# Performance work log

Measured on AMD Instinct MI355X. Metric: run time of the kernel, lower is better.

The kernel has to match this reference:

```python
import jax, jax.numpy as jnp
import numpy as np

B, T, I, H, O = 8192, 128, 28, 200, 10


def setup_inputs() -> dict:
    key = jax.random.key(0)
    ks = jax.random.split(key, 7)
    s_ih = 1.0 / np.sqrt(H)
    return {
        "x": jax.random.normal(ks[0], (B, T, I), dtype=jnp.float32),
        "W_ih": jax.random.uniform(ks[1], (H, I), jnp.float32, -s_ih, s_ih),
        "W_hh": jax.random.uniform(ks[2], (H, H), jnp.float32, -s_ih, s_ih),
        "b_ih": jax.random.uniform(ks[3], (H,), jnp.float32, -s_ih, s_ih),
        "b_hh": jax.random.uniform(ks[4], (H,), jnp.float32, -s_ih, s_ih),
        "W_fc": jax.random.uniform(ks[5], (O, H), jnp.float32, -s_ih, s_ih),
        "b_fc": jax.random.uniform(ks[6], (O,), jnp.float32, -s_ih, s_ih),
    }


def reference(x, W_ih, W_hh, b_ih, b_hh, W_fc, b_fc):
    # Precompute input projections for all timesteps in one GEMM: [B,T,H]
    xp = jnp.einsum("bti,hi->bth", x, W_ih) + b_ih + b_hh
    h0 = jnp.zeros((x.shape[0], W_hh.shape[0]), dtype=x.dtype)

    def step(h, xp_t):
        # h_t = relu(x_t W_ih^T + b_ih + h_{t-1} W_hh^T + b_hh)
        h = jax.nn.relu(xp_t + h @ W_hh.T)
        return h, None

    # scan over time: xp transposed to [T,B,H]
    h_last, _ = jax.lax.scan(step, h0, jnp.swapaxes(xp, 0, 1))
    # out[:, -1, :] then fc1
    return h_last @ W_fc.T + b_fc
```

## Files before the change

### kernel.cpp

```cpp
#include <hip/hip_runtime.h>
#include <hip/hip_bf16.h>

typedef float f4v __attribute__((ext_vector_type(4)));
typedef short s8v __attribute__((ext_vector_type(8)));

#define TT 128
#define II 28
#define HH 200
#define BB 16
#define NT 128
#define SH 232
#define KX 224
#define SF 212

__device__ __forceinline__ int pk_bf16(float a, float b) {
    union { __hip_bfloat162 h; int i; } u;
    u.h = __float22bfloat162_rn(make_float2(a, b));
    return u.i;
}
__device__ __forceinline__ short f2bf(float f) {
    union { __hip_bfloat16 h; short s; } u;
    u.h = __float2bfloat16(f);
    return u.s;
}

__global__ __launch_bounds__(NT, 1)
void rnn_w2(const float* __restrict__ x,
            const float* __restrict__ W_ih,
            const float* __restrict__ W_hh,
            const float* __restrict__ b_ih,
            const float* __restrict__ b_hh,
            const float* __restrict__ W_fc,
            const float* __restrict__ b_fc,
            float* __restrict__ out)
{
    __shared__ __align__(16) short Hs[2][BB][SH];
    __shared__ __align__(16) float Hf[BB][SF];

    const int tid  = threadIdx.x;
    const int lane = tid & 63;
    const int q    = lane >> 4;
    const int lr   = lane & 15;
    const int wave = tid >> 6;
    const int b0   = blockIdx.x * BB;

    const int first = wave * 7;
    const int cnt   = wave ? 6 : 7;

    for (int i = tid; i < 2 * BB * SH / 2; i += NT) ((int*)Hs)[i] = 0;

    s8v Af[7][8];
    #pragma unroll
    for (int u = 0; u < 7; ++u) {
        const int j = 16 * (first + u) + lr;
        #pragma unroll
        for (int kc = 0; kc < 8; ++kc) {
            union { short s[8]; s8v v; } tv;
            #pragma unroll
            for (int i = 0; i < 8; ++i) {
                const int k = 32 * kc + 8 * q + i;
                float w = 0.0f;
                if (u < cnt && j < HH) {
                    if (k < HH)                    w = W_hh[j * HH + k];
                    else if (k >= KX && k < KX+II) w = W_ih[j * II + (k - KX)];
                }
                tv.s[i] = f2bf(w);
            }
            Af[u][kc] = tv.v;
        }
    }

    f4v biasv[7];
    #pragma unroll
    for (int u = 0; u < 7; ++u) {
        f4v bv = {0.f, 0.f, 0.f, 0.f};
        #pragma unroll
        for (int i = 0; i < 4; ++i) {
            const int j = 16 * (first + u) + 4 * q + i;
            if (u < cnt && j < HH) bv[i] = b_ih[j] + b_hh[j];
        }
        biasv[u] = bv;
    }

    const float* xp = x + (long)(b0 + lr) * (TT * II) + 8 * q;
    f4v xa0 = {0,0,0,0}, xb0 = {0,0,0,0}, xa1 = {0,0,0,0}, xb1 = {0,0,0,0};
    xa0 = *(const f4v*)(xp);
    if (q != 3) xb0 = *(const f4v*)(xp + 4);
    xa1 = *(const f4v*)(xp + II);
    if (q != 3) xb1 = *(const f4v*)(xp + II + 4);

    __syncthreads();

    auto step = [&](int t, int pb, f4v& xa, f4v& xb) {
        union { int i4[4]; s8v v; } xf;
        xf.i4[0] = pk_bf16(xa.x, xa.y);
        xf.i4[1] = pk_bf16(xa.z, xa.w);
        xf.i4[2] = pk_bf16(xb.x, xb.y);
        xf.i4[3] = pk_bf16(xb.z, xb.w);
        {
            const int tn = (t + 2 < TT) ? t + 2 : TT - 1;
            xa = *(const f4v*)(xp + tn * II);
            if (q != 3) xb = *(const f4v*)(xp + tn * II + 4);
        }

        s8v bf[7];
        #pragma unroll
        for (int kc = 0; kc < 7; ++kc)
            bf[kc] = *(const s8v*)&Hs[pb][lr][32 * kc + 8 * q];

        #pragma unroll
        for (int u = 0; u < 7; ++u) {
            if (u < cnt) {
                const int jt = first + u;
                f4v acc = __builtin_amdgcn_mfma_f32_16x16x32_bf16(Af[u][7], xf.v, biasv[u], 0, 0, 0);
                #pragma unroll
                for (int kc = 0; kc < 7; ++kc)
                    acc = __builtin_amdgcn_mfma_f32_16x16x32_bf16(Af[u][kc], bf[kc], acc, 0, 0, 0);

                const float r0 = fmaxf(acc.x, 0.f), r1 = fmaxf(acc.y, 0.f);
                const float r2 = fmaxf(acc.z, 0.f), r3 = fmaxf(acc.w, 0.f);
                int2 hv;
                hv.x = pk_bf16(r0, r1);
                hv.y = pk_bf16(r2, r3);
                *(int2*)&Hs[pb ^ 1][lr][16 * jt + 4 * q] = hv;
                if (t == TT - 1) {
                    f4v rf = {r0, r1, r2, r3};
                    *(f4v*)&Hf[lr][16 * jt + 4 * q] = rf;
                }
            }
        }
        __syncthreads();
    };

    for (int tb = 0; tb < TT; tb += 2) {
        step(tb,     0, xa0, xb0);
        step(tb + 1, 1, xa1, xb1);
    }

    for (int i = tid; i < BB * 10; i += NT) {
        const int o = i >> 4, r = i & 15;
        float s = b_fc[o];
        for (int k = 0; k < HH; ++k)
            s = fmaf(Hf[r][k], W_fc[o * HH + k], s);
        __builtin_nontemporal_store(s, &out[(long)(b0 + r) * 10 + o]);
    }
}

extern "C" void kernel_launch(void* const* d_in, const int* in_sizes, int n_in,
                              void* d_out, int out_size, void* d_ws, size_t ws_size,
                              hipStream_t stream) {
    const float* x    = (const float*)d_in[0];
    const float* W_ih = (const float*)d_in[1];
    const float* W_hh = (const float*)d_in[2];
    const float* b_ih = (const float*)d_in[3];
    const float* b_hh = (const float*)d_in[4];
    const float* W_fc = (const float*)d_in[5];
    const float* b_fc = (const float*)d_in[6];
    float* out = (float*)d_out;

    rnn_w2<<<dim3(8192 / BB), dim3(NT), 0, stream>>>(
        x, W_ih, W_hh, b_ih, b_hh, W_fc, b_fc, out);
}
```

Measured before the change: 325.4 us.

## Interleave independent MFMA chains and prefetch x four timesteps ahead

The MFMA loop is reordered so that the seven output tiles' accumulators advance together across k-chunks, replacing seven serial dependent chains per tile. This hides MFMA latency between dependent instructions. The x prefetch changes from a 2-step lookahead to chunked 4-timestep double buffering, so global load latency is covered over several steps. Wave 1 now always computes the seventh tile, which is padding with zero weights, and simply skips storing it. This trades extra MFMA work and more registers for fewer stalls.

```diff
diff --git a/kernel.cpp b/kernel.cpp
--- a/kernel.cpp
+++ b/kernel.cpp
@@ -25,7 +25,7 @@
 }
 
 __global__ __launch_bounds__(NT, 1)
-void rnn_w2(const float* __restrict__ x,
+void rnn_w3(const float* __restrict__ x,
             const float* __restrict__ W_ih,
             const float* __restrict__ W_hh,
             const float* __restrict__ b_ih,
@@ -45,7 +45,6 @@
     const int b0   = blockIdx.x * BB;
 
     const int first = wave * 7;
-    const int cnt   = wave ? 6 : 7;
 
     for (int i = tid; i < 2 * BB * SH / 2; i += NT) ((int*)Hs)[i] = 0;
 
@@ -60,7 +59,7 @@
             for (int i = 0; i < 8; ++i) {
                 const int k = 32 * kc + 8 * q + i;
                 float w = 0.0f;
-                if (u < cnt && j < HH) {
+                if (j < HH) {
                     if (k < HH)                    w = W_hh[j * HH + k];
                     else if (k >= KX && k < KX+II) w = W_ih[j * II + (k - KX)];
                 }
@@ -77,48 +76,50 @@
         #pragma unroll
         for (int i = 0; i < 4; ++i) {
             const int j = 16 * (first + u) + 4 * q + i;
-            if (u < cnt && j < HH) bv[i] = b_ih[j] + b_hh[j];
+            if (j < HH) bv[i] = b_ih[j] + b_hh[j];
         }
         biasv[u] = bv;
     }
 
     const float* xp = x + (long)(b0 + lr) * (TT * II) + 8 * q;
-    f4v xa0 = {0,0,0,0}, xb0 = {0,0,0,0}, xa1 = {0,0,0,0}, xb1 = {0,0,0,0};
-    xa0 = *(const f4v*)(xp);
-    if (q != 3) xb0 = *(const f4v*)(xp + 4);
-    xa1 = *(const f4v*)(xp + II);
-    if (q != 3) xb1 = *(const f4v*)(xp + II + 4);
+    f4v xA[8] = {}, xB[8] = {};
+    #pragma unroll
+    for (int s = 0; s < 4; ++s) {
+        xA[2*s] = *(const f4v*)(xp + s * II);
+        if (q < 3) xA[2*s+1] = *(const f4v*)(xp + s * II + 4);
+    }
 
     __syncthreads();
 
-    auto step = [&](int t, int pb, f4v& xa, f4v& xb) {
+    auto step = [&](int t, int pb, const f4v& xa, const f4v& xb) {
+        s8v bf[7];
+        #pragma unroll
+        for (int kc = 0; kc < 7; ++kc)
+            bf[kc] = *(const s8v*)&Hs[pb][lr][32 * kc + 8 * q];
+
         union { int i4[4]; s8v v; } xf;
         xf.i4[0] = pk_bf16(xa.x, xa.y);
         xf.i4[1] = pk_bf16(xa.z, xa.w);
         xf.i4[2] = pk_bf16(xb.x, xb.y);
         xf.i4[3] = pk_bf16(xb.z, xb.w);
-        {
-            const int tn = (t + 2 < TT) ? t + 2 : TT - 1;
-            xa = *(const f4v*)(xp + tn * II);
-            if (q != 3) xb = *(const f4v*)(xp + tn * II + 4);
+
+        f4v acc[7];
+        #pragma unroll
+        for (int u = 0; u < 7; ++u)
+            acc[u] = __builtin_amdgcn_mfma_f32_16x16x32_bf16(Af[u][7], xf.v, biasv[u], 0, 0, 0);
+        #pragma unroll
+        for (int kc = 0; kc < 7; ++kc) {
+            #pragma unroll
+            for (int u = 0; u < 7; ++u)
+                acc[u] = __builtin_amdgcn_mfma_f32_16x16x32_bf16(Af[u][kc], bf[kc], acc[u], 0, 0, 0);
         }
-
-        s8v bf[7];
-        #pragma unroll
-        for (int kc = 0; kc < 7; ++kc)
-            bf[kc] = *(const s8v*)&Hs[pb][lr][32 * kc + 8 * q];
 
         #pragma unroll
         for (int u = 0; u < 7; ++u) {
-            if (u < cnt) {
+            if (u < 6 || wave == 0) {
                 const int jt = first + u;
-                f4v acc = __builtin_amdgcn_mfma_f32_16x16x32_bf16(Af[u][7], xf.v, biasv[u], 0, 0, 0);
-                #pragma unroll
-                for (int kc = 0; kc < 7; ++kc)
-                    acc = __builtin_amdgcn_mfma_f32_16x16x32_bf16(Af[u][kc], bf[kc], acc, 0, 0, 0);
-
-                const float r0 = fmaxf(acc.x, 0.f), r1 = fmaxf(acc.y, 0.f);
-                const float r2 = fmaxf(acc.z, 0.f), r3 = fmaxf(acc.w, 0.f);
+                const float r0 = fmaxf(acc[u].x, 0.f), r1 = fmaxf(acc[u].y, 0.f);
+                const float r2 = fmaxf(acc[u].z, 0.f), r3 = fmaxf(acc[u].w, 0.f);
                 int2 hv;
                 hv.x = pk_bf16(r0, r1);
                 hv.y = pk_bf16(r2, r3);
@@ -132,9 +133,22 @@
         __syncthreads();
     };
 
-    for (int tb = 0; tb < TT; tb += 2) {
-        step(tb,     0, xa0, xb0);
-        step(tb + 1, 1, xa1, xb1);
+    auto chunk = [&](int tc, f4v (&cur)[8], f4v (&nxt)[8]) {
+        if (tc + 4 < TT) {
+            #pragma unroll
+            for (int s = 0; s < 4; ++s) {
+                nxt[2*s] = *(const f4v*)(xp + (tc + 4 + s) * II);
+                if (q < 3) nxt[2*s+1] = *(const f4v*)(xp + (tc + 4 + s) * II + 4);
+            }
+        }
+        #pragma unroll
+        for (int s = 0; s < 4; ++s)
+            step(tc + s, (tc + s) & 1, cur[2*s], cur[2*s+1]);
+    };
+
+    for (int tc = 0; tc < TT; tc += 8) {
+        chunk(tc,     xA, xB);
+        chunk(tc + 4, xB, xA);
     }
 
     for (int i = tid; i < BB * 10; i += NT) {
@@ -158,6 +172,6 @@
     const float* b_fc = (const float*)d_in[6];
     float* out = (float*)d_out;
 
-    rnn_w2<<<dim3(8192 / BB), dim3(NT), 0, stream>>>(
+    rnn_w3<<<dim3(8192 / BB), dim3(NT), 0, stream>>>(
         x, W_ih, W_hh, b_ih, b_hh, W_fc, b_fc, out);
 }
```

Result: slower. 351.1 us (+7.9%).
